# Performance work log

Measured on AMD Instinct MI355X. Metric: run time of the kernel, lower is better.

## Reference

```python
import math
import jax, jax.numpy as jnp
import numpy as np

DIM = 4096
N_HEADS = 32
N_KV_HEADS = 8
HEAD_DIM = DIM // N_HEADS  # 128
N_REP = N_HEADS // N_KV_HEADS  # 4
BSZ = 1
SEQLEN = 2048
ROPE_THETA = 500000.0


def setup_inputs() -> dict:
    key = jax.random.key(0)
    ks = jax.random.split(key, 8)
    s = 1.0 / math.sqrt(DIM)
    x = jax.random.normal(ks[0], (BSZ, SEQLEN, DIM), dtype=jnp.float32)
    wq = jax.random.normal(ks[1], (DIM, N_HEADS * HEAD_DIM), dtype=jnp.float32) * s
    wk = jax.random.normal(ks[2], (DIM, N_KV_HEADS * HEAD_DIM), dtype=jnp.float32) * s
    wv = jax.random.normal(ks[3], (DIM, N_KV_HEADS * HEAD_DIM), dtype=jnp.float32) * s
    wo = jax.random.normal(ks[4], (N_HEADS * HEAD_DIM, DIM), dtype=jnp.float32) * s
    # RoPE frequencies: freqs_cis[t, j] = exp(i * t * theta^{-2j/hd})
    inv_freq = 1.0 / (ROPE_THETA ** (jnp.arange(0, HEAD_DIM, 2, dtype=jnp.float32) / HEAD_DIM))
    t = jnp.arange(SEQLEN, dtype=jnp.float32)
    angles = jnp.outer(t, inv_freq)  # [S, hd/2]
    freqs_cos = jnp.cos(angles)
    freqs_sin = jnp.sin(angles)
    # causal additive mask [S, S]: 0 on/below diagonal, -inf above
    mask = jnp.triu(jnp.full((SEQLEN, SEQLEN), float('-inf'), dtype=jnp.float32), k=1)
    cache_k = jnp.zeros((BSZ, SEQLEN, N_KV_HEADS, HEAD_DIM), dtype=jnp.float32)
    cache_v = jnp.zeros((BSZ, SEQLEN, N_KV_HEADS, HEAD_DIM), dtype=jnp.float32)
    return {"x": x, "wq": wq, "wk": wk, "wv": wv, "wo": wo,
            "freqs_cos": freqs_cos, "freqs_sin": freqs_sin, "mask": mask,
            "cache_k": cache_k, "cache_v": cache_v, "start_pos": 0}


def _apply_rotary(xq, xk, cos, sin):
    # xq: [B,S,Hq,hd], xk: [B,S,Hkv,hd]; cos/sin: [S, hd/2]
    def rot(x):
        b, s, h, d = x.shape
        xr = x.reshape(b, s, h, d // 2, 2)
        a, bb = xr[..., 0], xr[..., 1]
        c = cos[None, :, None, :]
        sn = sin[None, :, None, :]
        out = jnp.stack([a * c - bb * sn, a * sn + bb * c], axis=-1)
        return out.reshape(b, s, h, d)
    return rot(xq), rot(xk)


def reference(x, wq, wk, wv, wo, freqs_cos, freqs_sin, mask, cache_k, cache_v, start_pos):
    bsz, seqlen, _ = x.shape
    xq = (x @ wq).reshape(bsz, seqlen, N_HEADS, HEAD_DIM)
    xk = (x @ wk).reshape(bsz, seqlen, N_KV_HEADS, HEAD_DIM)
    xv = (x @ wv).reshape(bsz, seqlen, N_KV_HEADS, HEAD_DIM)
    xq, xk = _apply_rotary(xq, xk, freqs_cos, freqs_sin)
    # KV-cache append
    cache_k = jax.lax.dynamic_update_slice(cache_k, xk, (0, start_pos, 0, 0))
    cache_v = jax.lax.dynamic_update_slice(cache_v, xv, (0, start_pos, 0, 0))
    kv_len = start_pos + seqlen
    keys = cache_k[:, :kv_len]    # [B, T, Hkv, hd]
    values = cache_v[:, :kv_len]
    # GQA repeat (logical; einsum reshaping keeps math identical)
    keys = jnp.repeat(keys, N_REP, axis=2)      # [B, T, Hq, hd]
    values = jnp.repeat(values, N_REP, axis=2)
    scale = 1.0 / math.sqrt(HEAD_DIM)
    scores = jnp.einsum('bqhd,bkhd->bhqk', xq, keys) * scale
    scores = scores + mask[None, None, :, :kv_len]
    probs = jax.nn.softmax(scores.astype(jnp.float32), axis=-1).astype(xq.dtype)
    out = jnp.einsum('bhqk,bkhd->bqhd', probs, values)
    out = out.reshape(bsz, seqlen, N_HEADS * HEAD_DIM)
    return out @ wo
```

## Files before the change

### kernel.cpp

```cpp
#include <hip/hip_runtime.h>
#include <hip/hip_bf16.h>

typedef unsigned short u16;
typedef short short8 __attribute__((ext_vector_type(8)));
typedef float floatx4 __attribute__((ext_vector_type(4)));

#define DIM 4096
#define SEQ 2048
#define NH 32
#define NKV 8
#define HD 128
#define QKV_N 6144

static __device__ __forceinline__ float b2f(u16 u) {
    return __uint_as_float(((unsigned int)u) << 16);
}
static __device__ __forceinline__ u16 f2b(float f) {
    unsigned int u = __float_as_uint(f);
    u = (u + 0x7FFFu + ((u >> 16) & 1u)) >> 16;
    return (u16)u;
}
static __device__ __forceinline__ void async16(const u16* g, u16* l) {
    __builtin_amdgcn_global_load_lds((const __attribute__((address_space(1))) void*)g,
                                     (__attribute__((address_space(3))) void*)l, 16, 0, 0);
}

__global__ __launch_bounds__(256) void transpose_f32_bf16(const float* __restrict__ src,
                                                          u16* __restrict__ dst,
                                                          int R, int C) {
    __shared__ u16 tile[32][33];
    int c0 = blockIdx.x * 32, r0 = blockIdx.y * 32;
    int x = threadIdx.x & 31, y0 = threadIdx.x >> 5;
#pragma unroll
    for (int i = 0; i < 4; i++) {
        int r = y0 + i * 8;
        tile[r][x] = f2b(src[(size_t)(r0 + r) * C + c0 + x]);
    }
    __syncthreads();
#pragma unroll
    for (int i = 0; i < 4; i++) {
        int r = y0 + i * 8;
        dst[(size_t)(c0 + r) * R + r0 + x] = tile[x][r];
    }
}

__global__ __launch_bounds__(256) void convert_f32_bf16(const float* __restrict__ src,
                                                        u16* __restrict__ dst) {
    int i = (blockIdx.x * 256 + threadIdx.x) * 4;
    float4 f = *(const float4*)(src + i);
    ushort4 o;
    o.x = f2b(f.x); o.y = f2b(f.y); o.z = f2b(f.z); o.w = f2b(f.w);
    *(ushort4*)(dst + i) = o;
}

__global__ __launch_bounds__(256) void transpose_v(const u16* __restrict__ Xqkv,
                                                   u16* __restrict__ VT) {
    __shared__ u16 tile[32][33];
    int k0 = blockIdx.x * 32, d0 = blockIdx.y * 32, h = blockIdx.z;
    const u16* src = Xqkv + DIM + NKV * HD + h * HD;
    int x = threadIdx.x & 31, y0 = threadIdx.x >> 5;
#pragma unroll
    for (int i = 0; i < 4; i++) {
        int r = y0 + i * 8;
        tile[r][x] = src[(size_t)(k0 + r) * QKV_N + d0 + x];
    }
    __syncthreads();
    u16* dst = VT + ((size_t)h * HD + d0) * SEQ + k0;
#pragma unroll
    for (int i = 0; i < 4; i++) {
        int r = y0 + i * 8;
        dst[(size_t)r * SEQ + x] = tile[x][r];
    }
}

template<bool CF32>
__global__ __launch_bounds__(256) void gemm_bf16(const u16* __restrict__ A,
                                                 const u16* __restrict__ Bt,
                                                 void* __restrict__ Cv,
                                                 int M, int N, int K) {
    __shared__ u16 As[128 * 32];
    __shared__ u16 Bs[128 * 32];
    int tid = threadIdx.x;
    int wave = tid >> 6, lane = tid & 63, quad = lane >> 4, l16 = lane & 15;
    int wrow = (wave >> 1) * 64, wcol = (wave & 1) * 64;
    int m0 = blockIdx.y * 128, n0 = blockIdx.x * 128;

    int g = (lane & 3) ^ ((lane >> 3) & 3);
    int srow = lane >> 2;
    const u16* Ap = A + (size_t)(m0 + wave * 32 + srow) * K + g * 8;
    const u16* Bp = Bt + (size_t)(n0 + wave * 32 + srow) * K + g * 8;
    u16* As0 = &As[wave * 1024];
    u16* Bs0 = &Bs[wave * 1024];
    int sA = quad ^ ((l16 >> 1) & 3);

    floatx4 acc[4][4];
#pragma unroll
    for (int i = 0; i < 4; i++)
#pragma unroll
        for (int j = 0; j < 4; j++) acc[i][j] = (floatx4){0.f, 0.f, 0.f, 0.f};

    int nk = K >> 5;
    for (int kb = 0; kb < nk; kb++) {
        __syncthreads();
        const u16* a0 = Ap + kb * 32;
        const u16* b0 = Bp + kb * 32;
        async16(a0, As0);
        async16(a0 + (size_t)16 * K, As0 + 512);
        async16(b0, Bs0);
        async16(b0 + (size_t)16 * K, Bs0 + 512);
        __syncthreads();
        short8 a[4], b[4];
#pragma unroll
        for (int mt = 0; mt < 4; mt++)
            a[mt] = *(const short8*)&As[(wrow + mt * 16 + l16) * 32 + sA * 8];
#pragma unroll
        for (int nt = 0; nt < 4; nt++)
            b[nt] = *(const short8*)&Bs[(wcol + nt * 16 + l16) * 32 + sA * 8];
#pragma unroll
        for (int mt = 0; mt < 4; mt++)
#pragma unroll
            for (int nt = 0; nt < 4; nt++)
                acc[mt][nt] = __builtin_amdgcn_mfma_f32_16x16x32_bf16(a[mt], b[nt], acc[mt][nt], 0, 0, 0);
    }

#pragma unroll
    for (int mt = 0; mt < 4; mt++)
#pragma unroll
        for (int nt = 0; nt < 4; nt++) {
            int row = m0 + wrow + mt * 16 + quad * 4;
            int col = n0 + wcol + nt * 16 + l16;
#pragma unroll
            for (int r = 0; r < 4; r++) {
                if constexpr (CF32)
                    ((float*)Cv)[(size_t)(row + r) * N + col] = acc[mt][nt][r];
                else
                    ((u16*)Cv)[(size_t)(row + r) * N + col] = f2b(acc[mt][nt][r]);
            }
        }
}

__global__ __launch_bounds__(256) void rope_kernel(u16* __restrict__ X,
                                                   const float* __restrict__ fc,
                                                   const float* __restrict__ fs) {
    int idx = blockIdx.x * 256 + threadIdx.x;
    int i = idx & 63;
    int rem = idx >> 6;
    int h = rem % 40;
    int pos = rem / 40;
    int col = (h < 32) ? (h * 128 + 2 * i) : (4096 + (h - 32) * 128 + 2 * i);
    size_t off = (size_t)pos * QKV_N + col;
    unsigned int pr = *(unsigned int*)&X[off];
    float a = b2f((u16)(pr & 0xffffu));
    float b = b2f((u16)(pr >> 16));
    float c = fc[pos * 64 + i];
    float s = fs[pos * 64 + i];
    float na = a * c - b * s;
    float nb = a * s + b * c;
    unsigned int outw = ((unsigned int)f2b(nb) << 16) | (unsigned int)f2b(na);
    *(unsigned int*)&X[off] = outw;
}

__global__ __launch_bounds__(256) void attn_kernel(const u16* __restrict__ Xqkv,
                                                   const u16* __restrict__ VT,
                                                   u16* __restrict__ O) {
    __shared__ u16 Ks[64 * 128];
    __shared__ u16 Vt[128 * 64];
    __shared__ u16 Ps[4 * 1024];
    int head = blockIdx.y;
    int kvh = head >> 2;
    const u16* Xq = Xqkv + head * HD;
    const u16* Xk = Xqkv + DIM + kvh * HD;
    const u16* Vg = VT + (size_t)kvh * HD * SEQ;
    int tid = threadIdx.x, wave = tid >> 6, lane = tid & 63, quad = lane >> 4, l16 = lane & 15;

    size_t offKe = (size_t)quad * QKV_N + (size_t)((l16 ^ quad) * 8);
    size_t offKo = (size_t)quad * QKV_N + (size_t)((l16 ^ (quad + 4)) * 8);
    size_t offV  = (size_t)(lane >> 3) * SEQ + (size_t)((((lane & 7) ^ ((lane >> 3) & 7))) * 8);
    int sK[4];
#pragma unroll
    for (int ks = 0; ks < 4; ks++) sK[ks] = (ks * 4 + quad) ^ (l16 & 7);

    const float scale = 0.08838834764831845f;

    for (int pass = 0; pass < 2; pass++) {
        int qb = pass ? (31 - blockIdx.x) : blockIdx.x;
        int q0 = qb * 64;

        short8 aq[4];
        {
            const u16* qp = Xq + (size_t)(q0 + wave * 16 + l16) * QKV_N + quad * 8;
#pragma unroll
            for (int ks = 0; ks < 4; ks++) aq[ks] = *(const short8*)(qp + ks * 32);
        }
        float l_i[4] = {0.f, 0.f, 0.f, 0.f};
        floatx4 o_acc[8];
#pragma unroll
        for (int i = 0; i < 8; i++) o_acc[i] = (floatx4){0.f, 0.f, 0.f, 0.f};

        for (int kb = 0; kb <= qb; kb++) {
            __syncthreads();
#pragma unroll
            for (int c = 0; c < 4; c++) {
                int kc = wave * 4 + c;
                const u16* gp = Xk + (size_t)(kb * 64 + kc * 4) * QKV_N + ((kc & 1) ? offKo : offKe);
                async16(gp, &Ks[kc * 512]);
            }
#pragma unroll
            for (int c = 0; c < 4; c++) {
                int vc = wave * 4 + c;
                async16(Vg + (size_t)(vc * 8) * SEQ + (size_t)(kb * 64) + offV, &Vt[vc * 512]);
            }
            __syncthreads();

            floatx4 s[4];
#pragma unroll
            for (int nt = 0; nt < 4; nt++) s[nt] = (floatx4){0.f, 0.f, 0.f, 0.f};
#pragma unroll
            for (int ks = 0; ks < 4; ks++) {
#pragma unroll
                for (int nt = 0; nt < 4; nt++) {
                    short8 bk = *(const short8*)&Ks[(nt * 16 + l16) * 128 + sK[ks] * 8];
                    s[nt] = __builtin_amdgcn_mfma_f32_16x16x32_bf16(aq[ks], bk, s[nt], 0, 0, 0);
                }
            }

            bool diag = (kb == qb);
            int qrel = wave * 16 + quad * 4;
            float rowsum[4] = {0.f, 0.f, 0.f, 0.f};
#pragma unroll
            for (int nt = 0; nt < 4; nt++) {
                int kcol = nt * 16 + l16;
#pragma unroll
                for (int r = 0; r < 4; r++) {
                    float v = s[nt][r] * scale;
                    if (diag && kcol > qrel + r) v = -__builtin_inff();
                    float p = __expf(fminf(v, 60.f));
                    s[nt][r] = p;
                    rowsum[r] += p;
                }
            }
#pragma unroll
            for (int m = 1; m < 16; m <<= 1)
#pragma unroll
                for (int r = 0; r < 4; r++)
                    rowsum[r] += __shfl_xor(rowsum[r], m);
#pragma unroll
            for (int r = 0; r < 4; r++) l_i[r] += rowsum[r];

            u16* pw = &Ps[wave * 1024];
#pragma unroll
            for (int nt = 0; nt < 4; nt++) {
                int gbase = nt * 2 + (l16 >> 3);
#pragma unroll
                for (int r = 0; r < 4; r++) {
                    int row = quad * 4 + r;
                    int slot = gbase ^ (row & 7);
                    unsigned u = __float_as_uint(s[nt][r]);
                    pw[row * 64 + slot * 8 + (l16 & 7)] = (u16)((u + 0x8000u) >> 16);
                }
            }

#pragma unroll
            for (int ks = 0; ks < 2; ks++) {
                short8 ap = *(const short8*)&Ps[wave * 1024 + l16 * 64 + sK[ks] * 8];
#pragma unroll
                for (int nt = 0; nt < 8; nt++) {
                    short8 bv = *(const short8*)&Vt[(nt * 16 + l16) * 64 + sK[ks] * 8];
                    o_acc[nt] = __builtin_amdgcn_mfma_f32_16x16x32_bf16(ap, bv, o_acc[nt], 0, 0, 0);
                }
            }
        }

        float invl[4];
#pragma unroll
        for (int r = 0; r < 4; r++) invl[r] = 1.f / l_i[r];
#pragma unroll
        for (int nt = 0; nt < 8; nt++) {
            int row = q0 + wave * 16 + quad * 4;
            int col = head * HD + nt * 16 + l16;
#pragma unroll
            for (int r = 0; r < 4; r++)
                O[(size_t)(row + r) * DIM + col] = f2b(o_acc[nt][r] * invl[r]);
        }
    }
}

extern "C" void kernel_launch(void* const* d_in, const int* in_sizes, int n_in,
                              void* d_out, int out_size, void* d_ws, size_t ws_size,
                              hipStream_t stream) {
    const float* x  = (const float*)d_in[0];
    const float* wq = (const float*)d_in[1];
    const float* wk = (const float*)d_in[2];
    const float* wv = (const float*)d_in[3];
    const float* wo = (const float*)d_in[4];
    const float* fc = (const float*)d_in[5];
    const float* fs = (const float*)d_in[6];

    u16* WT   = (u16*)d_ws;
    u16* Xqkv = WT + (size_t)QKV_N * DIM;
    u16* Obuf = Xqkv + (size_t)SEQ * QKV_N;
    u16* xbf  = Obuf;
    u16* VT   = WT + (size_t)5120 * DIM;
    float* outp = (float*)d_out;

    transpose_f32_bf16<<<dim3(128, 128), 256, 0, stream>>>(wq, WT, 4096, 4096);
    transpose_f32_bf16<<<dim3(32, 128), 256, 0, stream>>>(wk, WT + (size_t)4096 * 4096, 4096, 1024);
    transpose_f32_bf16<<<dim3(32, 128), 256, 0, stream>>>(wv, WT + (size_t)5120 * 4096, 4096, 1024);

    convert_f32_bf16<<<(SEQ * DIM) / 1024, 256, 0, stream>>>(x, xbf);

    gemm_bf16<false><<<dim3(QKV_N / 128, SEQ / 128), 256, 0, stream>>>(xbf, WT, Xqkv, SEQ, QKV_N, DIM);

    rope_kernel<<<(SEQ * 40 * 64) / 256, 256, 0, stream>>>(Xqkv, fc, fs);

    transpose_v<<<dim3(SEQ / 32, HD / 32, NKV), 256, 0, stream>>>(Xqkv, VT);

    attn_kernel<<<dim3(16, NH), 256, 0, stream>>>(Xqkv, VT, Obuf);

    transpose_f32_bf16<<<dim3(128, 128), 256, 0, stream>>>(wo, WT, 4096, 4096);

    gemm_bf16<true><<<dim3(DIM / 128, SEQ / 128), 256, 0, stream>>>(Obuf, WT, outp, SEQ, DIM, DIM);
}
```

Measured before the change: 557.7 us.

## Replace GEMM with 4-stage async-LDS pipelined kernel with XCD-aware tile mapping

Swaps the single-buffered 128x128 bf16 GEMM for a 512-thread kernel with 256-wide N tiles and a 4-deep ring of LDS buffers filled by async global-to-LDS loads three k-steps ahead. It uses explicit vmcnt waits and raw barriers instead of two syncthreads per step. Workgroups are remapped so consecutive tiles land on the same XCD, and MFMA sections get raised wave priority. The aim is to hide global load latency and improve L2 reuse, at the cost of more LDS and registers per block. The projection GEMMs use MR=8 for QKV and MR=4 for the output.

```diff
diff --git a/kernel.cpp b/kernel.cpp
--- a/kernel.cpp
+++ b/kernel.cpp
@@ -73,68 +73,107 @@
     }
 }
 
-template<bool CF32>
-__global__ __launch_bounds__(256) void gemm_bf16(const u16* __restrict__ A,
-                                                 const u16* __restrict__ Bt,
-                                                 void* __restrict__ Cv,
-                                                 int M, int N, int K) {
-    __shared__ u16 As[128 * 32];
-    __shared__ u16 Bs[128 * 32];
+template<int MR, bool CF32>
+__global__ __launch_bounds__(512, 2) void gemm_pipe(const u16* __restrict__ A,
+                                                    const u16* __restrict__ Bt,
+                                                    void* __restrict__ Cv,
+                                                    int M, int N, int K) {
+    constexpr int BM = MR * 32;
+    constexpr int BN = 256;
+    constexpr int TILE = (BM + BN) * 32;
+    constexpr int ACALLS = MR / 4;
+    constexpr int LPP = ACALLS + 2;
+
+    __shared__ __align__(128) u16 lds[4 * TILE];
+
     int tid = threadIdx.x;
     int wave = tid >> 6, lane = tid & 63, quad = lane >> 4, l16 = lane & 15;
-    int wrow = (wave >> 1) * 64, wcol = (wave & 1) * 64;
-    int m0 = blockIdx.y * 128, n0 = blockIdx.x * 128;
-
+    int wm = wave >> 2, wn = wave & 3;
+
+    int nwg = gridDim.x;
+    int NT = N >> 8;
+    int orig = blockIdx.x;
+    int q = nwg >> 3, r = nwg & 7;
+    int xcd = orig & 7, idx = orig >> 3;
+    int wg = (xcd < r ? xcd * (q + 1) : r * (q + 1) + (xcd - r) * q) + idx;
+    int m0 = (wg / NT) * BM, n0 = (wg % NT) * BN;
+
+    int srow = lane >> 2;
     int g = (lane & 3) ^ ((lane >> 3) & 3);
-    int srow = lane >> 2;
-    const u16* Ap = A + (size_t)(m0 + wave * 32 + srow) * K + g * 8;
+    const u16* Ap = A + (size_t)(m0 + wave * (MR * 4) + srow) * K + g * 8;
     const u16* Bp = Bt + (size_t)(n0 + wave * 32 + srow) * K + g * 8;
-    u16* As0 = &As[wave * 1024];
-    u16* Bs0 = &Bs[wave * 1024];
-    int sA = quad ^ ((l16 >> 1) & 3);
-
-    floatx4 acc[4][4];
-#pragma unroll
-    for (int i = 0; i < 4; i++)
+    int sA = (quad ^ ((l16 >> 1) & 3)) * 8;
+
+    floatx4 acc[MR][4];
+#pragma unroll
+    for (int i = 0; i < MR; i++)
 #pragma unroll
         for (int j = 0; j < 4; j++) acc[i][j] = (floatx4){0.f, 0.f, 0.f, 0.f};
 
-    int nk = K >> 5;
-    for (int kb = 0; kb < nk; kb++) {
-        __syncthreads();
-        const u16* a0 = Ap + kb * 32;
-        const u16* b0 = Bp + kb * 32;
-        async16(a0, As0);
-        async16(a0 + (size_t)16 * K, As0 + 512);
-        async16(b0, Bs0);
-        async16(b0 + (size_t)16 * K, Bs0 + 512);
-        __syncthreads();
-        short8 a[4], b[4];
-#pragma unroll
-        for (int mt = 0; mt < 4; mt++)
-            a[mt] = *(const short8*)&As[(wrow + mt * 16 + l16) * 32 + sA * 8];
+    auto stage = [&](int t) {
+        int buf = t & 3;
+        const u16* a0 = Ap + (size_t)t * 32;
+        const u16* b0 = Bp + (size_t)t * 32;
+        u16* as = lds + buf * TILE + wave * (MR * 128);
+        u16* bs = lds + buf * TILE + BM * 32 + wave * 1024;
+#pragma unroll
+        for (int c = 0; c < ACALLS; c++)
+            async16(a0 + (size_t)(c * 16) * K, as + c * 512);
+#pragma unroll
+        for (int c = 0; c < 2; c++)
+            async16(b0 + (size_t)(c * 16) * K, bs + c * 512);
+    };
+
+    auto compute = [&](int t) {
+        int buf = t & 3;
+        const u16* Ab = lds + buf * TILE;
+        const u16* Bb = Ab + BM * 32;
+        short8 a[MR], b[4];
+#pragma unroll
+        for (int mt = 0; mt < MR; mt++)
+            a[mt] = *(const short8*)&Ab[(wm * (MR * 16) + mt * 16 + l16) * 32 + sA];
 #pragma unroll
         for (int nt = 0; nt < 4; nt++)
-            b[nt] = *(const short8*)&Bs[(wcol + nt * 16 + l16) * 32 + sA * 8];
-#pragma unroll
-        for (int mt = 0; mt < 4; mt++)
+            b[nt] = *(const short8*)&Bb[(wn * 64 + nt * 16 + l16) * 32 + sA];
+        __builtin_amdgcn_s_setprio(1);
+#pragma unroll
+        for (int mt = 0; mt < MR; mt++)
 #pragma unroll
             for (int nt = 0; nt < 4; nt++)
                 acc[mt][nt] = __builtin_amdgcn_mfma_f32_16x16x32_bf16(a[mt], b[nt], acc[mt][nt], 0, 0, 0);
-    }
-
-#pragma unroll
-    for (int mt = 0; mt < 4; mt++)
+        __builtin_amdgcn_s_setprio(0);
+    };
+
+    int nk = K >> 5;
+    stage(0); stage(1); stage(2);
+    asm volatile("s_waitcnt vmcnt(%0)" :: "n"(2 * LPP) : "memory");
+    __builtin_amdgcn_s_barrier();
+    for (int t = 0; t < nk - 3; t++) {
+        stage(t + 3);
+        compute(t);
+        asm volatile("s_waitcnt vmcnt(%0)" :: "n"(2 * LPP) : "memory");
+        __builtin_amdgcn_s_barrier();
+    }
+    compute(nk - 3);
+    asm volatile("s_waitcnt vmcnt(%0)" :: "n"(LPP) : "memory");
+    __builtin_amdgcn_s_barrier();
+    compute(nk - 2);
+    asm volatile("s_waitcnt vmcnt(0)" ::: "memory");
+    __builtin_amdgcn_s_barrier();
+    compute(nk - 1);
+
+#pragma unroll
+    for (int mt = 0; mt < MR; mt++)
 #pragma unroll
         for (int nt = 0; nt < 4; nt++) {
-            int row = m0 + wrow + mt * 16 + quad * 4;
-            int col = n0 + wcol + nt * 16 + l16;
-#pragma unroll
-            for (int r = 0; r < 4; r++) {
+            int row = m0 + wm * (MR * 16) + mt * 16 + quad * 4;
+            int col = n0 + wn * 64 + nt * 16 + l16;
+#pragma unroll
+            for (int rr = 0; rr < 4; rr++) {
                 if constexpr (CF32)
-                    ((float*)Cv)[(size_t)(row + r) * N + col] = acc[mt][nt][r];
+                    ((float*)Cv)[(size_t)(row + rr) * N + col] = acc[mt][nt][rr];
                 else
-                    ((u16*)Cv)[(size_t)(row + r) * N + col] = f2b(acc[mt][nt][r]);
+                    ((u16*)Cv)[(size_t)(row + rr) * N + col] = f2b(acc[mt][nt][rr]);
             }
         }
 }
@@ -309,7 +348,7 @@
 
     convert_f32_bf16<<<(SEQ * DIM) / 1024, 256, 0, stream>>>(x, xbf);
 
-    gemm_bf16<false><<<dim3(QKV_N / 128, SEQ / 128), 256, 0, stream>>>(xbf, WT, Xqkv, SEQ, QKV_N, DIM);
+    gemm_pipe<8, false><<<dim3(192), 512, 0, stream>>>(xbf, WT, Xqkv, SEQ, QKV_N, DIM);
 
     rope_kernel<<<(SEQ * 40 * 64) / 256, 256, 0, stream>>>(Xqkv, fc, fs);
 
@@ -319,5 +358,5 @@
 
     transpose_f32_bf16<<<dim3(128, 128), 256, 0, stream>>>(wo, WT, 4096, 4096);
 
-    gemm_bf16<true><<<dim3(DIM / 128, SEQ / 128), 256, 0, stream>>>(Obuf, WT, outp, SEQ, DIM, DIM);
-}
+    gemm_pipe<4, true><<<dim3(256), 512, 0, stream>>>(Obuf, WT, outp, SEQ, DIM, DIM);
+}
```

Measured after the change: 513.1 us. 1.09x faster.
